# Kernel optimization log

Measured on AMD Instinct MI355X. Metric: run time of the kernel, lower is better.

The kernel has to match this reference:

```python
import jax, jax.numpy as jnp
import numpy as np

N_ITER = 4
D = 768  # word_emb_dim == sent_dim of both CrossAttentionBlocks


def setup_inputs() -> dict:
    key = jax.random.key(0)
    ks = jax.random.split(key, 6)
    N_S, N_F = 16384, 4096
    return {
        "sents_emb": jax.random.normal(ks[0], (N_S, D), jnp.float32),
        "func_embed": jax.random.normal(ks[1], (N_F, D), jnp.float32),
        "Wv_f2s": jax.random.normal(ks[2], (D, D), jnp.float32) * 0.02,
        "bv_f2s": jax.random.normal(ks[3], (D,), jnp.float32) * 0.02,
        "Wv_s2f": jax.random.normal(ks[4], (D, D), jnp.float32) * 0.02,
        "bv_s2f": jax.random.normal(ks[5], (D,), jnp.float32) * 0.02,
    }


def reference(sents_emb, func_embed, Wv_f2s, bv_f2s, Wv_s2f, bv_s2f):
    scale = 1.0 / jnp.sqrt(jnp.asarray(D, sents_emb.dtype))
    sents_hid, func_hid = sents_emb, func_embed
    z = None
    for _ in range(N_ITER):  # small fixed iteration count, sequential dependency
        # func2sent: query=sents_hid, key=func_hid, value=W_v(func_hid)
        func_val = func_hid @ Wv_f2s.T + bv_f2s              # [N_f, D]
        z = scale * (sents_hid @ func_hid.T)                  # [N_s, N_f] logits (returned)
        att = jax.nn.softmax(z, axis=1)
        sents_hid = sents_hid + att @ func_val                # [N_s, D]
        # sent2func: query=func_hid, key=sents_hid, value=W_v(sents_hid)
        sent_val = sents_hid @ Wv_s2f.T + bv_s2f              # [N_s, D]
        z2 = scale * (func_hid @ sents_hid.T)                 # [N_f, N_s]
        func_hid = func_hid + jax.nn.softmax(z2, axis=1) @ sent_val
    return (sents_hid, func_hid, z)
```

## Files before the change

kernel.cpp:

```cpp
#include <hip/hip_runtime.h>
#include <stdint.h>

typedef __attribute__((ext_vector_type(8))) short s16x8;
typedef __attribute__((ext_vector_type(8))) unsigned short u16x8;
typedef __attribute__((ext_vector_type(4))) unsigned short u16x4;
typedef __attribute__((ext_vector_type(4))) float f32x4;

__device__ inline unsigned short f2b(float f){
  unsigned u = __builtin_bit_cast(unsigned, f);
  u = u + 0x7fffu + ((u >> 16) & 1u);
  return (unsigned short)(u >> 16);
}
__device__ inline float b2f(unsigned short h){
  unsigned u = ((unsigned)h) << 16;
  return __builtin_bit_cast(float, u);
}

typedef __attribute__((address_space(1))) const unsigned g_uint;
typedef __attribute__((address_space(3))) unsigned l_uint;

__device__ inline void gload_lds16(const void* g, void* l){
  __builtin_amdgcn_global_load_lds((g_uint*)reinterpret_cast<uintptr_t>(g),
                                   (l_uint*)reinterpret_cast<uintptr_t>(l), 16, 0, 0);
}

#define BARF() { __builtin_amdgcn_s_barrier(); asm volatile("" ::: "memory"); }
#define LGKM0() { asm volatile("s_waitcnt lgkmcnt(0)" ::: "memory"); }

__device__ inline unsigned xcd_swizzle(unsigned lin, unsigned tot){
  const unsigned q = tot >> 3;
  return (lin & 7) * q + (lin >> 3);
}

template<int EPI>
__global__ __launch_bounds__(512, 2) void gemm256(
    const unsigned short* __restrict__ A, const unsigned short* __restrict__ B,
    int M, int N, int K, float scale,
    float* __restrict__ Cf, unsigned short* __restrict__ Cb,
    float* __restrict__ lsum)
{
  __shared__ __align__(16) char ldsraw[131072];
  const int tid  = threadIdx.x;
  const int wid  = tid >> 6, lane = tid & 63;
  const int wm   = wid >> 2, wn = wid & 3;

  const unsigned gx = gridDim.x, gy = gridDim.y;
  const unsigned lin = blockIdx.x + gx*blockIdx.y;
  const unsigned w   = xcd_swizzle(lin, gx*gy);
  const int bm = (w / gx) * 256, bn = (w % gx) * 256;

  const int NT = K >> 6;

  f32x4 acc[8][4] = {};

  auto stageA = [&](int T, int halfm){
    const int kb = T << 6;
    char* ldsb = ldsraw + ((T & 1) << 16) + halfm*16384;
    #pragma unroll
    for (int i = 0; i < 2; ++i){
      const int lr  = i*64 + (tid >> 3);
      const int gtr = halfm*64 + ((lr < 64) ? lr : lr + 64);
      const int sc  = ((tid & 7)*8) ^ ((lr & 7)*8);
      gload_lds16(A + (size_t)(bm + gtr)*K + kb + sc, ldsb + i*8192 + tid*16);
    }
  };
  auto stageB = [&](int T, int halfk){
    const int kb = (T << 6) + halfk*32;
    char* ldsb = ldsraw + ((T & 1) << 16) + 32768 + halfk*16384;
    #pragma unroll
    for (int i = 0; i < 2; ++i){
      const int lr = i*128 + (tid >> 2);
      const int sc = ((tid & 3)*8) ^ ((lr & 3)*8);
      gload_lds16(B + (size_t)(bn + lr)*K + kb + sc, ldsb + i*8192 + tid*16);
    }
  };

  const int fr = lane & 15;
  const int fo = (lane >> 4) << 4;
  const int amask = (fr & 7) << 4;
  const int bmask = (fr & 3) << 4;

  auto rdA = [&](const char* ldsS, int mh, int kk, s16x8* af){
    const char* ab = ldsS + mh*16384;
    #pragma unroll
    for (int mf = 0; mf < 4; ++mf){
      const int r = wm*64 + mf*16 + fr;
      af[mf] = *(const s16x8*)(ab + r*128 + ((kk*64 + fo) ^ amask));
    }
  };
  auto rdB = [&](const char* ldsS, int kk, s16x8* bf){
    const char* bb = ldsS + 32768 + kk*16384;
    #pragma unroll
    for (int nf = 0; nf < 4; ++nf){
      const int r = wn*64 + nf*16 + fr;
      bf[nf] = *(const s16x8*)(bb + r*64 + (fo ^ bmask));
    }
  };

  stageB(0, 0); stageA(0, 0); stageA(0, 1); stageB(0, 1);
  stageB(1, 0); stageA(1, 0);
  asm volatile("s_waitcnt vmcnt(4)" ::: "memory");
  BARF();

  for (int T = 0; T < NT; ++T){
    const char* ldsS = ldsraw + ((T & 1) << 16);
    s16x8 af[4], bf[4];
    rdA(ldsS, 0, 0, af); rdB(ldsS, 0, bf);
    if (T + 1 < NT) stageA(T + 1, 1);
    BARF();
    __builtin_amdgcn_s_setprio(1);
    #pragma unroll
    for (int mf = 0; mf < 4; ++mf)
      #pragma unroll
      for (int nf = 0; nf < 4; ++nf)
        acc[mf][nf] = __builtin_amdgcn_mfma_f32_16x16x32_bf16(af[mf], bf[nf], acc[mf][nf], 0, 0, 0);
    __builtin_amdgcn_s_setprio(0);
    BARF();
    rdA(ldsS, 1, 0, af);
    if (T + 1 < NT) stageB(T + 1, 1);
    BARF();
    __builtin_amdgcn_s_setprio(1);
    #pragma unroll
    for (int mf = 0; mf < 4; ++mf)
      #pragma unroll
      for (int nf = 0; nf < 4; ++nf)
        acc[4 + mf][nf] = __builtin_amdgcn_mfma_f32_16x16x32_bf16(af[mf], bf[nf], acc[4 + mf][nf], 0, 0, 0);
    __builtin_amdgcn_s_setprio(0);
    BARF();
    rdA(ldsS, 0, 1, af); rdB(ldsS, 1, bf);
    if (T + 2 < NT) stageB(T + 2, 0);
    BARF();
    __builtin_amdgcn_s_setprio(1);
    #pragma unroll
    for (int mf = 0; mf < 4; ++mf)
      #pragma unroll
      for (int nf = 0; nf < 4; ++nf)
        acc[mf][nf] = __builtin_amdgcn_mfma_f32_16x16x32_bf16(af[mf], bf[nf], acc[mf][nf], 0, 0, 0);
    __builtin_amdgcn_s_setprio(0);
    BARF();
    rdA(ldsS, 1, 1, af);
    if (T + 2 < NT) stageA(T + 2, 0);
    BARF();
    __builtin_amdgcn_s_setprio(1);
    #pragma unroll
    for (int mf = 0; mf < 4; ++mf)
      #pragma unroll
      for (int nf = 0; nf < 4; ++nf)
        acc[4 + mf][nf] = __builtin_amdgcn_mfma_f32_16x16x32_bf16(af[mf], bf[nf], acc[4 + mf][nf], 0, 0, 0);
    __builtin_amdgcn_s_setprio(0);
    if (T < NT - 2) { asm volatile("s_waitcnt vmcnt(4)" ::: "memory"); }
    else            { asm volatile("s_waitcnt vmcnt(0)" ::: "memory"); }
    BARF();
  }

  char* wlds = ldsraw + wid*16384;
  const int hi = lane >> 4;
  #pragma unroll
  for (int mf = 0; mf < 8; ++mf){
    #pragma unroll
    for (int j = 0; j < 4; ++j){
      const int rl = mf*16 + hi*4 + j;
      #pragma unroll
      for (int nf = 0; nf < 4; ++nf){
        const float zz = acc[mf][nf][j] * scale;
        if (EPI == 6){
          const int row = bm + wm*128 + rl;
          const int col = bn + wn*64 + fr + nf*16;
          Cf[(size_t)row * N + col] = zz;
        }
        const int cl = fr + nf*16;
        *(unsigned short*)(wlds + rl*128 + ((cl*2) ^ (((rl>>2)&3) << 5))) = f2b(__expf(zz));
      }
    }
  }
  LGKM0();

  float rs16[16];
  const int g8 = lane >> 3;
  #pragma unroll
  for (int t = 0; t < 16; ++t){
    const u16x8 v = *(const u16x8*)(wlds + t*1024 + lane*16);
    const int rl = t*8 + g8;
    const int c0 = (((lane & 7)*16) ^ (((rl>>2)&3) << 5)) >> 1;
    const int row = bm + wm*128 + rl;
    *(u16x8*)(Cb + (size_t)row * N + bn + wn*64 + c0) = v;
    float s = 0.f;
    #pragma unroll
    for (int k = 0; k < 8; ++k) s += b2f(v[k]);
    s += __shfl_xor(s, 1, 64); s += __shfl_xor(s, 2, 64); s += __shfl_xor(s, 4, 64);
    rs16[t] = s;
  }
  __syncthreads();
  float* lds_rs = (float*)ldsraw;
  if (tid < 256) lds_rs[tid] = 0.f;
  __syncthreads();
  if ((lane & 7) == 0){
    #pragma unroll
    for (int t = 0; t < 16; ++t)
      atomicAdd(&lds_rs[wm*128 + t*8 + g8], rs16[t]);
  }
  __syncthreads();
  if (tid < 256) atomicAdd(&lsum[bm + tid], lds_rs[tid]);
}

template<int EPI>
__global__ __launch_bounds__(256, 4) void gemm_bt(
    const unsigned short* __restrict__ A, const unsigned short* __restrict__ B,
    int M, int N, int KS, float scale, const float* __restrict__ bias,
    const float* __restrict__ lsum,
    float* __restrict__ Cf, unsigned short* __restrict__ Cb)
{
  __shared__ __align__(16) char ldsb[32768];
  unsigned short* As = (unsigned short*)ldsb;
  unsigned short* Bs = As + 128*64;
  const int tid  = threadIdx.x;
  const int wid  = tid >> 6, lane = tid & 63;
  const int wr   = wid >> 1, wc = wid & 1;

  const unsigned gx = gridDim.x, gy = gridDim.y;
  const unsigned lin = blockIdx.x + gx*(blockIdx.y + gy*blockIdx.z);
  const unsigned w   = xcd_swizzle(lin, gx*gy*gridDim.z);
  const unsigned bxs = w % gx;
  const unsigned rest = w / gx;
  const unsigned bys = rest % gy;
  const unsigned bzs = rest / gy;

  const int bm   = bys * 128, bn = bxs * 128;
  const int kb   = bzs * KS, ke = kb + KS;

  f32x4 acc[4][4] = {};

  const int l8   = lane >> 3;
  const int scol = ((((lane & 7) << 4) ^ (l8 << 4)) >> 1);
  const int Klead = gridDim.z * KS;

  const unsigned short* Ag[4]; const unsigned short* Bg[4];
  unsigned short* Al[4]; unsigned short* Bl[4];
  #pragma unroll
  for (int i = 0; i < 4; ++i){
    const int row = wid*32 + i*8 + l8;
    Ag[i] = A + (size_t)(bm + row) * Klead + scol;
    Bg[i] = B + (size_t)(bn + row) * Klead + scol;
    Al[i] = As + (wid*4 + i) * 512;
    Bl[i] = Bs + (wid*4 + i) * 512;
  }

  const int fr    = lane & 15;
  const int fk    = (lane >> 4) << 4;
  const int amask = (fr & 7) << 4;

  for (int k0 = kb; k0 < ke; k0 += 64){
    if (k0 != kb) __syncthreads();
    #pragma unroll
    for (int i = 0; i < 4; ++i){
      gload_lds16(Ag[i] + k0, Al[i]);
      gload_lds16(Bg[i] + k0, Bl[i]);
    }
    __syncthreads();
    #pragma unroll
    for (int kk = 0; kk < 2; ++kk){
      s16x8 af[4], bf[4];
      #pragma unroll
      for (int m = 0; m < 4; ++m){
        const int row = (wr << 6) + m*16 + fr;
        const int off = row*128 + (((kk << 6) + fk) ^ amask);
        af[m] = *(const s16x8*)((const char*)As + off);
      }
      #pragma unroll
      for (int n = 0; n < 4; ++n){
        const int row = (wc << 6) + n*16 + fr;
        const int off = row*128 + (((kk << 6) + fk) ^ amask);
        bf[n] = *(const s16x8*)((const char*)Bs + off);
      }
      #pragma unroll
      for (int m = 0; m < 4; ++m)
        #pragma unroll
        for (int n = 0; n < 4; ++n)
          acc[m][n] = __builtin_amdgcn_mfma_f32_16x16x32_bf16(af[m], bf[n], acc[m][n], 0, 0, 0);
    }
  }
  __syncthreads();

  char* wlds = ldsb + wid*8192;
  const int hi = lane >> 4;
  const size_t pbase = (size_t)bzs * M * N;
  #pragma unroll
  for (int mh = 0; mh < 2; ++mh){
    #pragma unroll
    for (int ms = 0; ms < 2; ++ms){
      #pragma unroll
      for (int j = 0; j < 4; ++j){
        const int rl = ms*16 + hi*4 + j;
        #pragma unroll
        for (int n = 0; n < 4; ++n){
          const int cl = fr + n*16;
          *(float*)(wlds + rl*256 + ((cl*4) ^ (((rl>>2)&3) << 5))) = acc[mh*2 + ms][n][j];
        }
      }
    }
    LGKM0();
    #pragma unroll
    for (int t = 0; t < 8; ++t){
      const f32x4 d = *(const f32x4*)(wlds + t*1024 + lane*16);
      const int rl = t*4 + hi;
      const int c0 = (((lane & 15)*16) ^ (((rl>>2)&3) << 5)) >> 2;
      const int row = bm + (wr << 6) + mh*32 + rl;
      const int col = bn + (wc << 6) + c0;
      const size_t idx = (size_t)row * N + col;
      if (EPI == 2){
        const float bi = bias[row];
        u16x4 o; o[0]=f2b(d[0]+bi); o[1]=f2b(d[1]+bi); o[2]=f2b(d[2]+bi); o[3]=f2b(d[3]+bi);
        *(u16x4*)(Cb + idx) = o;
      } else if (EPI == 4){
        *(f32x4*)(Cf + pbase + idx) = d;
      } else {
        const float li = 1.0f / lsum[row];
        f32x4 o = *(const f32x4*)(Cf + idx);
        o += d * li;
        *(f32x4*)(Cf + idx) = o;
        u16x4 ob; ob[0]=f2b(o[0]); ob[1]=f2b(o[1]); ob[2]=f2b(o[2]); ob[3]=f2b(o[3]);
        *(u16x4*)(Cb + idx) = ob;
      }
    }
    LGKM0();
  }
}

__global__ __launch_bounds__(256) void reduce_splitk(
    const float* __restrict__ P, int S, size_t stride4,
    const float* __restrict__ lsum, int d4,
    float* __restrict__ Cf, unsigned short* __restrict__ Cb, int n4)
{
  const int i = blockIdx.x * 256 + threadIdx.x;
  if (i >= n4) return;
  f32x4 s = {0.f, 0.f, 0.f, 0.f};
  for (int k = 0; k < S; ++k) s += ((const f32x4*)P)[(size_t)k * stride4 + i];
  const float li = 1.0f / lsum[i / d4];
  f32x4 r = ((const f32x4*)Cf)[i];
  r += s * li;
  ((f32x4*)Cf)[i] = r;
  u16x4 o;
  o[0] = f2b(r[0]); o[1] = f2b(r[1]); o[2] = f2b(r[2]); o[3] = f2b(r[3]);
  ((u16x4*)Cb)[i] = o;
}

__global__ void cvt8(const float* __restrict__ src, float* __restrict__ dstf,
                     unsigned short* __restrict__ dstb, int n8)
{
  const int i = blockIdx.x * 256 + threadIdx.x;
  if (i >= n8) return;
  const f32x4 a = ((const f32x4*)src)[2*i];
  const f32x4 b = ((const f32x4*)src)[2*i + 1];
  if (dstf){ ((f32x4*)dstf)[2*i] = a; ((f32x4*)dstf)[2*i + 1] = b; }
  u16x8 o;
  o[0]=f2b(a[0]); o[1]=f2b(a[1]); o[2]=f2b(a[2]); o[3]=f2b(a[3]);
  o[4]=f2b(b[0]); o[5]=f2b(b[1]); o[6]=f2b(b[2]); o[7]=f2b(b[3]);
  ((u16x8*)dstb)[i] = o;
}

extern "C" void kernel_launch(void* const* d_in, const int* in_sizes, int n_in,
                              void* d_out, int out_size, void* d_ws, size_t ws_size,
                              hipStream_t stream)
{
  (void)in_sizes; (void)n_in; (void)out_size; (void)ws_size;
  const float* sents = (const float*)d_in[0];
  const float* funcs = (const float*)d_in[1];
  const float* WvA   = (const float*)d_in[2];
  const float* bvA   = (const float*)d_in[3];
  const float* WvB   = (const float*)d_in[4];
  const float* bvB   = (const float*)d_in[5];

  const int NS = 16384, NF = 4096, D = 768;

  float* outS = (float*)d_out;
  float* outF = outS + (size_t)NS * D;
  float* outZ = outF + (size_t)NF * D;

  char* ws = (char*)d_ws;
  unsigned short* att = (unsigned short*)ws;  ws += (size_t)NS * NF * 2;
  unsigned short* z2  = att;
  unsigned short* sb  = (unsigned short*)ws;  ws += (size_t)NS * D * 2;
  unsigned short* fb  = (unsigned short*)ws;  ws += (size_t)NF * D * 2;
  unsigned short* fvT = (unsigned short*)ws;  ws += (size_t)D * NF * 2;
  unsigned short* svT = (unsigned short*)ws;  ws += (size_t)D * NS * 2;
  unsigned short* wA  = (unsigned short*)ws;  ws += (size_t)D * D * 2;
  unsigned short* wB  = (unsigned short*)ws;  ws += (size_t)D * D * 2;
  float* lsum = (float*)ws;  ws += (size_t)NS * 4;
  float* Pbuf = (float*)ws;  ws += (size_t)NF * D * 4 * 4;

  const float scale = 0.036084391824351615f;

  cvt8<<<dim3((NS*D/8 + 255)/256), 256, 0, stream>>>(sents, outS, sb, NS*D/8);
  cvt8<<<dim3((NF*D/8 + 255)/256), 256, 0, stream>>>(funcs, outF, fb, NF*D/8);
  cvt8<<<dim3((D*D/8 + 255)/256),  256, 0, stream>>>(WvA, nullptr, wA, D*D/8);
  cvt8<<<dim3((D*D/8 + 255)/256),  256, 0, stream>>>(WvB, nullptr, wB, D*D/8);

  for (int it = 0; it < 4; ++it){
    gemm_bt<2><<<dim3(NF/128, D/128, 1), dim3(256), 0, stream>>>(wA, fb, D, NF, D, 0.f, bvA, nullptr, nullptr, fvT);
    hipMemsetAsync(lsum, 0, NS*4, stream);
    if (it < 3){
      gemm256<5><<<dim3(NF/256, NS/256), dim3(512), 0, stream>>>(sb, fb, NS, NF, D, scale, nullptr, att, lsum);
    } else {
      gemm256<6><<<dim3(NF/256, NS/256), dim3(512), 0, stream>>>(sb, fb, NS, NF, D, scale, outZ, att, lsum);
    }
    gemm_bt<7><<<dim3(D/128, NS/128, 1), dim3(256), 0, stream>>>(att, fvT, NS, D, NF, 0.f, nullptr, lsum, outS, sb);
    gemm_bt<2><<<dim3(NS/128, D/128, 1), dim3(256), 0, stream>>>(wB, sb, D, NS, D, 0.f, bvB, nullptr, nullptr, svT);
    hipMemsetAsync(lsum, 0, NF*4, stream);
    gemm256<5><<<dim3(NS/256, NF/256), dim3(512), 0, stream>>>(fb, sb, NF, NS, D, scale, nullptr, z2, lsum);
    gemm_bt<4><<<dim3(D/128, NF/128, 4), dim3(256), 0, stream>>>(z2, svT, NF, D, 4096, 0.f, nullptr, nullptr, Pbuf, nullptr);
    reduce_splitk<<<dim3(NF*D/4/256), 256, 0, stream>>>(Pbuf, 4, (size_t)NF*D/4, lsum, D/4, outF, fb, NF*D/4);
  }
}
```

Before: 2.196 ms.

## Restructure 256x256 GEMM mainloop into two half-K phases with unified staging

Reorganizes the gemm256 main loop from four quarter-phases (split over M halves and K halves) into two phases over K halves. Each phase loads all 8 A fragments and 4 B fragments and issues 32 MFMAs, using one staging lambda and one LDS swizzle for both operands. This halves the barriers per K tile and lengthens MFMA runs between them. The cost is more live fragment registers (8 A fragments) and a deeper outstanding-load count. Separately, it splits the row-sum buffer into two and merges the two per-iteration memsets into one.

```diff
diff --git a/kernel.cpp b/kernel.cpp
--- a/kernel.cpp
+++ b/kernel.cpp
@@ -53,39 +53,27 @@
 
   f32x4 acc[8][4] = {};
 
-  auto stageA = [&](int T, int halfm){
-    const int kb = T << 6;
-    char* ldsb = ldsraw + ((T & 1) << 16) + halfm*16384;
-    #pragma unroll
-    for (int i = 0; i < 2; ++i){
-      const int lr  = i*64 + (tid >> 3);
-      const int gtr = halfm*64 + ((lr < 64) ? lr : lr + 64);
-      const int sc  = ((tid & 7)*8) ^ ((lr & 7)*8);
-      gload_lds16(A + (size_t)(bm + gtr)*K + kb + sc, ldsb + i*8192 + tid*16);
-    }
-  };
-  auto stageB = [&](int T, int halfk){
-    const int kb = (T << 6) + halfk*32;
-    char* ldsb = ldsraw + ((T & 1) << 16) + 32768 + halfk*16384;
+  auto stageU = [&](int T, int reg, const unsigned short* P, int prow){
+    char* base = ldsraw + ((T & 1) << 16) + reg*16384;
+    const int kb = (T << 6) + (reg & 1)*32;
     #pragma unroll
     for (int i = 0; i < 2; ++i){
       const int lr = i*128 + (tid >> 2);
-      const int sc = ((tid & 3)*8) ^ ((lr & 3)*8);
-      gload_lds16(B + (size_t)(bn + lr)*K + kb + sc, ldsb + i*8192 + tid*16);
+      const int sc = ((tid & 3)*8) ^ (((lr >> 1) & 3)*8);
+      gload_lds16(P + (size_t)(prow + lr)*K + kb + sc, base + i*8192 + tid*16);
     }
   };
 
   const int fr = lane & 15;
   const int fo = (lane >> 4) << 4;
-  const int amask = (fr & 7) << 4;
-  const int bmask = (fr & 3) << 4;
-
-  auto rdA = [&](const char* ldsS, int mh, int kk, s16x8* af){
-    const char* ab = ldsS + mh*16384;
-    #pragma unroll
-    for (int mf = 0; mf < 4; ++mf){
-      const int r = wm*64 + mf*16 + fr;
-      af[mf] = *(const s16x8*)(ab + r*128 + ((kk*64 + fo) ^ amask));
+  const int xm = ((fr >> 1) & 3) << 4;
+
+  auto rdA = [&](const char* ldsS, int kk, s16x8* af){
+    const char* ab = ldsS + kk*16384;
+    #pragma unroll
+    for (int mf = 0; mf < 8; ++mf){
+      const int r = wm*128 + mf*16 + fr;
+      af[mf] = *(const s16x8*)(ab + r*64 + (fo ^ (((r >> 1) & 3) << 4)));
     }
   };
   auto rdB = [&](const char* ldsS, int kk, s16x8* bf){
@@ -93,62 +81,44 @@
     #pragma unroll
     for (int nf = 0; nf < 4; ++nf){
       const int r = wn*64 + nf*16 + fr;
-      bf[nf] = *(const s16x8*)(bb + r*64 + (fo ^ bmask));
+      bf[nf] = *(const s16x8*)(bb + r*64 + (fo ^ (((r >> 1) & 3) << 4)));
     }
   };
-
-  stageB(0, 0); stageA(0, 0); stageA(0, 1); stageB(0, 1);
-  stageB(1, 0); stageA(1, 0);
-  asm volatile("s_waitcnt vmcnt(4)" ::: "memory");
+  (void)xm;
+
+  stageU(0, 0, A, bm); stageU(0, 2, B, bn);
+  stageU(0, 1, A, bm); stageU(0, 3, B, bn);
+  stageU(1, 0, A, bm); stageU(1, 2, B, bn);
+  asm volatile("s_waitcnt vmcnt(8)" ::: "memory");
   BARF();
 
   for (int T = 0; T < NT; ++T){
     const char* ldsS = ldsraw + ((T & 1) << 16);
-    s16x8 af[4], bf[4];
-    rdA(ldsS, 0, 0, af); rdB(ldsS, 0, bf);
-    if (T + 1 < NT) stageA(T + 1, 1);
+    s16x8 af[8], bf[4];
+    rdA(ldsS, 0, af); rdB(ldsS, 0, bf);
+    if (T + 1 < NT){ stageU(T + 1, 1, A, bm); stageU(T + 1, 3, B, bn); }
     BARF();
     __builtin_amdgcn_s_setprio(1);
     #pragma unroll
-    for (int mf = 0; mf < 4; ++mf)
+    for (int mf = 0; mf < 8; ++mf)
       #pragma unroll
       for (int nf = 0; nf < 4; ++nf)
         acc[mf][nf] = __builtin_amdgcn_mfma_f32_16x16x32_bf16(af[mf], bf[nf], acc[mf][nf], 0, 0, 0);
     __builtin_amdgcn_s_setprio(0);
+    if (T < NT - 2) { asm volatile("s_waitcnt vmcnt(8)" ::: "memory"); }
+    else            { asm volatile("s_waitcnt vmcnt(0)" ::: "memory"); }
     BARF();
-    rdA(ldsS, 1, 0, af);
-    if (T + 1 < NT) stageB(T + 1, 1);
+    rdA(ldsS, 1, af); rdB(ldsS, 1, bf);
+    if (T + 2 < NT){ stageU(T + 2, 0, A, bm); stageU(T + 2, 2, B, bn); }
     BARF();
     __builtin_amdgcn_s_setprio(1);
     #pragma unroll
-    for (int mf = 0; mf < 4; ++mf)
-      #pragma unroll
-      for (int nf = 0; nf < 4; ++nf)
-        acc[4 + mf][nf] = __builtin_amdgcn_mfma_f32_16x16x32_bf16(af[mf], bf[nf], acc[4 + mf][nf], 0, 0, 0);
-    __builtin_amdgcn_s_setprio(0);
-    BARF();
-    rdA(ldsS, 0, 1, af); rdB(ldsS, 1, bf);
-    if (T + 2 < NT) stageB(T + 2, 0);
-    BARF();
-    __builtin_amdgcn_s_setprio(1);
-    #pragma unroll
-    for (int mf = 0; mf < 4; ++mf)
+    for (int mf = 0; mf < 8; ++mf)
       #pragma unroll
       for (int nf = 0; nf < 4; ++nf)
         acc[mf][nf] = __builtin_amdgcn_mfma_f32_16x16x32_bf16(af[mf], bf[nf], acc[mf][nf], 0, 0, 0);
     __builtin_amdgcn_s_setprio(0);
-    BARF();
-    rdA(ldsS, 1, 1, af);
-    if (T + 2 < NT) stageA(T + 2, 0);
-    BARF();
-    __builtin_amdgcn_s_setprio(1);
-    #pragma unroll
-    for (int mf = 0; mf < 4; ++mf)
-      #pragma unroll
-      for (int nf = 0; nf < 4; ++nf)
-        acc[4 + mf][nf] = __builtin_amdgcn_mfma_f32_16x16x32_bf16(af[mf], bf[nf], acc[4 + mf][nf], 0, 0, 0);
-    __builtin_amdgcn_s_setprio(0);
-    if (T < NT - 2) { asm volatile("s_waitcnt vmcnt(4)" ::: "memory"); }
+    if (T < NT - 2) { asm volatile("s_waitcnt vmcnt(8)" ::: "memory"); }
     else            { asm volatile("s_waitcnt vmcnt(0)" ::: "memory"); }
     BARF();
   }
@@ -385,7 +355,8 @@
   unsigned short* svT = (unsigned short*)ws;  ws += (size_t)D * NS * 2;
   unsigned short* wA  = (unsigned short*)ws;  ws += (size_t)D * D * 2;
   unsigned short* wB  = (unsigned short*)ws;  ws += (size_t)D * D * 2;
-  float* lsum = (float*)ws;  ws += (size_t)NS * 4;
+  float* lsumS = (float*)ws;  ws += (size_t)NS * 4;
+  float* lsumF = (float*)ws;  ws += (size_t)NF * 4;
   float* Pbuf = (float*)ws;  ws += (size_t)NF * D * 4 * 4;
 
   const float scale = 0.036084391824351615f;
@@ -396,18 +367,17 @@
   cvt8<<<dim3((D*D/8 + 255)/256),  256, 0, stream>>>(WvB, nullptr, wB, D*D/8);
 
   for (int it = 0; it < 4; ++it){
+    hipMemsetAsync(lsumS, 0, (NS + NF)*4, stream);
     gemm_bt<2><<<dim3(NF/128, D/128, 1), dim3(256), 0, stream>>>(wA, fb, D, NF, D, 0.f, bvA, nullptr, nullptr, fvT);
-    hipMemsetAsync(lsum, 0, NS*4, stream);
     if (it < 3){
-      gemm256<5><<<dim3(NF/256, NS/256), dim3(512), 0, stream>>>(sb, fb, NS, NF, D, scale, nullptr, att, lsum);
+      gemm256<5><<<dim3(NF/256, NS/256), dim3(512), 0, stream>>>(sb, fb, NS, NF, D, scale, nullptr, att, lsumS);
     } else {
-      gemm256<6><<<dim3(NF/256, NS/256), dim3(512), 0, stream>>>(sb, fb, NS, NF, D, scale, outZ, att, lsum);
-    }
-    gemm_bt<7><<<dim3(D/128, NS/128, 1), dim3(256), 0, stream>>>(att, fvT, NS, D, NF, 0.f, nullptr, lsum, outS, sb);
+      gemm256<6><<<dim3(NF/256, NS/256), dim3(512), 0, stream>>>(sb, fb, NS, NF, D, scale, outZ, att, lsumS);
+    }
+    gemm_bt<7><<<dim3(D/128, NS/128, 1), dim3(256), 0, stream>>>(att, fvT, NS, D, NF, 0.f, nullptr, lsumS, outS, sb);
     gemm_bt<2><<<dim3(NS/128, D/128, 1), dim3(256), 0, stream>>>(wB, sb, D, NS, D, 0.f, bvB, nullptr, nullptr, svT);
-    hipMemsetAsync(lsum, 0, NF*4, stream);
-    gemm256<5><<<dim3(NS/256, NF/256), dim3(512), 0, stream>>>(fb, sb, NF, NS, D, scale, nullptr, z2, lsum);
+    gemm256<5><<<dim3(NS/256, NF/256), dim3(512), 0, stream>>>(fb, sb, NF, NS, D, scale, nullptr, z2, lsumF);
     gemm_bt<4><<<dim3(D/128, NF/128, 4), dim3(256), 0, stream>>>(z2, svT, NF, D, 4096, 0.f, nullptr, nullptr, Pbuf, nullptr);
-    reduce_splitk<<<dim3(NF*D/4/256), 256, 0, stream>>>(Pbuf, 4, (size_t)NF*D/4, lsum, D/4, outF, fb, NF*D/4);
-  }
-}
+    reduce_splitk<<<dim3(NF*D/4/256), 256, 0, stream>>>(Pbuf, 4, (size_t)NF*D/4, lsumF, D/4, outF, fb, NF*D/4);
+  }
+}
```

New measurement: 2.216 ms. No clear change (+0.9%).
